# Kernel optimization log

Measured on AMD Instinct MI355X. Metric: run time of the kernel, lower is better.

The kernel has to match this reference:

```python
import jax, jax.numpy as jnp
import numpy as np

MAX_ONSET_DELAY_SAMPLES = 10


def apply_delays(templates, delays):
    # templates: (E, F, L), delays: (E, F) -> shifted templates with zero fill
    E, F, L = templates.shape
    d = jnp.round(jnp.clip(delays, -MAX_ONSET_DELAY_SAMPLES, MAX_ONSET_DELAY_SAMPLES)).astype(jnp.int32)
    idx = jnp.arange(L)                                   # (L,)
    src = idx[None, None, :] - d[:, :, None]              # (E, F, L) source index for torch.roll(shift=d)
    valid = (src >= 0) & (src < L)                        # zero out wrapped-around region
    src_c = jnp.clip(src, 0, L - 1)
    shifted = jnp.take_along_axis(templates, src_c, axis=2)
    return jnp.where(valid, shifted, jnp.zeros((), templates.dtype))


def setup_inputs() -> dict:
    key = jax.random.key(0)
    k1, k2, k3 = jax.random.split(key, 3)
    B, S, F = 64, 32768, 6
    E, L = 16, 80
    x = jax.random.normal(k1, (B, S, F), dtype=jnp.float32)
    templates = jax.random.normal(k2, (E, F, L), dtype=jnp.float32) * 0.1
    onset_delays = jax.random.normal(k3, (E, F), dtype=jnp.float32)
    return {"x": x, "templates": templates, "onset_delays": onset_delays}


def reference(x, templates, onset_delays):
    # x: (B, S, F); templates: (E, F, L); onset_delays: (E, F) -> scores (B, S, E)
    B, S, F = x.shape
    E, _, L = templates.shape
    delayed = apply_delays(templates, onset_delays)       # (E, F, L)
    kern = jnp.flip(delayed, axis=2)                      # torch flips template before conv1d
    pad = (L - 1) // 2
    # Fuse the 96 per-(event,feature) conv1d calls into one conv: sum over features
    # is exactly the input-channel contraction of a dense conv1d (in=F, out=E).
    score = jax.lax.conv_general_dilated(
        jnp.transpose(x, (0, 2, 1)),                      # (B, F, S)
        kern,                                             # (E, F, L) as OIH
        window_strides=(1,),
        padding=[(pad, pad)],
        dimension_numbers=("NCH", "OIH", "NCH"),
    )                                                     # (B, E, S_out)
    S_out = score.shape[2]
    if S_out > S:
        score = score[:, :, :S]
    elif S_out < S:
        score = jnp.pad(score, ((0, 0), (0, 0), (0, S - S_out)))
    return jnp.transpose(score, (0, 2, 1)) / (L * F)      # (B, S, E)
```

## Files before the change

### kernel.cpp

```cpp
#include <hip/hip_runtime.h>

#define BB 64
#define SS 32768
#define FF 6
#define EE 16
#define LL 80
#define KK 480
#define NSL 15
#define TBLK 256
#define NPHI 4
#define WROW 332
#define WUNITS 166

typedef _Float16 half8 __attribute__((ext_vector_type(8)));
typedef float f32x4 __attribute__((ext_vector_type(4)));

__global__ void prep_kernel(const float* __restrict__ tpl, const float* __restrict__ dly,
                            _Float16* __restrict__ wrev) {
    int n = blockIdx.x * 256 + threadIdx.x;
    if (n >= EE * KK) return;
    int e = n / KK, k = n - e * KK;
    int f = k / LL, r = k - f * LL;
    int m = LL - 1 - r;
    float dl = fminf(fmaxf(dly[e * FF + f], -10.f), 10.f);
    int d = (int)rintf(dl);
    int src = m - d;
    float v = (src >= 0 && src < LL) ? tpl[(e * FF + f) * LL + src] : 0.f;
    wrev[n] = (_Float16)v;
}

template <bool FROM_WS>
__global__ __launch_bounds__(256, 4) void corr_kernel(
    const float* __restrict__ x, const float* __restrict__ tpl,
    const float* __restrict__ dly, const _Float16* __restrict__ wrev,
    float* __restrict__ out) {
    __shared__ alignas(16) _Float16 xs[NPHI][FF][WROW];

    int tid = threadIdx.x;
    int b = blockIdx.x >> 7;
    int t0 = (blockIdx.x & 127) << 8;

    int lane = tid & 63;
    int wid = tid >> 6;
    int e = lane & 15;
    int g = lane >> 4;

    const float* xb = x + (size_t)b * (SS * FF);
    for (int it = tid; it < NPHI * WUNITS; it += 256) {
        int phi = it / WUNITS;
        int i = (it - phi * WUNITS) * 2;
        int pos = t0 + phi - 39 + i;
        float va[12];
        if (pos >= 0 && pos <= SS - 2) {
            const float* xp = xb + (size_t)pos * FF;
            #pragma unroll
            for (int q = 0; q < 6; q++)
                *(float2*)&va[2 * q] = *(const float2*)&xp[2 * q];
        } else {
            #pragma unroll
            for (int q = 0; q < 2; q++) {
                int p = pos + q;
                bool ok = (p >= 0) && (p < SS);
                #pragma unroll
                for (int f = 0; f < FF; f++)
                    va[q * 6 + f] = ok ? xb[(size_t)p * FF + f] : 0.f;
            }
        }
        #pragma unroll
        for (int f = 0; f < FF; f++) {
#if __has_builtin(__builtin_amdgcn_cvt_pkrtz)
            __fp16 __attribute__((ext_vector_type(2))) hp =
                __builtin_amdgcn_cvt_pkrtz(va[f], va[6 + f]);
            *(decltype(hp)*)&xs[phi][f][i] = hp;
#else
            xs[phi][f][i] = (_Float16)va[f];
            xs[phi][f][i + 1] = (_Float16)va[6 + f];
#endif
        }
    }

    f32x4 bqv[NSL];
    if constexpr (FROM_WS) {
        #pragma unroll
        for (int s = 0; s < NSL; s++)
            bqv[s] = *(const f32x4*)&wrev[e * KK + 32 * s + 8 * g];
    } else {
        __shared__ _Float16 Wlds[EE * KK];
        for (int n = tid; n < EE * KK; n += 256) {
            int ee = n / KK, k = n - ee * KK;
            int f = k / LL, r = k - f * LL;
            int m = LL - 1 - r;
            float dl = fminf(fmaxf(dly[ee * FF + f], -10.f), 10.f);
            int d = (int)rintf(dl);
            int src = m - d;
            float v = (src >= 0 && src < LL) ? tpl[(ee * FF + f) * LL + src] : 0.f;
            Wlds[n] = (_Float16)v;
        }
        __syncthreads();
        #pragma unroll
        for (int s = 0; s < NSL; s++)
            bqv[s] = *(const f32x4*)&Wlds[e * KK + 32 * s + 8 * g];
    }
    #pragma unroll
    for (int s = 0; s < NSL; s++)
        asm volatile("" : "+v"(bqv[s]));

    __syncthreads();

    int phi = wid;
    const char* xph = (const char*)&xs[phi][0][0];
    f32x4 acc[4];
    #pragma unroll
    for (int tt = 0; tt < 4; tt++) acc[tt] = (f32x4){0.f, 0.f, 0.f, 0.f};

    #pragma unroll
    for (int tt = 0; tt < 4; tt++) {
        int R = tt * 16 + (lane & 15);
        #pragma unroll
        for (int s = 0; s < NSL; s++) {
            int k0 = 32 * s + 8 * g;
            int f = (k0 * 205) >> 14;
            int r0 = k0 - 80 * f;
            const char* p = xph + 2 * (f * WROW + 4 * R + r0);
            uint2 lo = *(const uint2*)p;
            uint2 hi = *(const uint2*)(p + 8);
            union { unsigned u[4]; half8 h; } av;
            av.u[0] = lo.x; av.u[1] = lo.y; av.u[2] = hi.x; av.u[3] = hi.y;
            union { f32x4 f4; half8 h; } bv;
            bv.f4 = bqv[s];
            acc[tt] = __builtin_amdgcn_mfma_f32_16x16x32_f16(av.h, bv.h, acc[tt], 0, 0, 0);
        }
    }

    #pragma unroll
    for (int tt = 0; tt < 4; tt++) {
        #pragma unroll
        for (int j = 0; j < 4; j++) {
            int row = tt * 16 + g * 4 + j;
            int t = t0 + phi + 4 * row;
            float v = acc[tt][j] * (1.0f / 480.0f);
            if (t == SS - 1) v = 0.f;
            out[((size_t)b * SS + t) * EE + e] = v;
        }
    }
}

extern "C" void kernel_launch(void* const* d_in, const int* in_sizes, int n_in,
                              void* d_out, int out_size, void* d_ws, size_t ws_size,
                              hipStream_t stream) {
    const float* x = (const float*)d_in[0];
    const float* tpl = (const float*)d_in[1];
    const float* dly = (const float*)d_in[2];
    float* out = (float*)d_out;

    int grid = BB * (SS / TBLK);
    if (ws_size >= (size_t)(EE * KK * sizeof(_Float16))) {
        _Float16* wrev = (_Float16*)d_ws;
        prep_kernel<<<(EE * KK + 255) / 256, 256, 0, stream>>>(tpl, dly, wrev);
        corr_kernel<true><<<grid, 256, 0, stream>>>(x, tpl, dly, wrev, out);
    } else {
        corr_kernel<false><<<grid, 256, 0, stream>>>(x, tpl, dly, nullptr, out);
    }
}
```

Before: 68.26 us.

## Process four time tiles per block with per-wave private staging, no block barriers

Each block now covers 1024 time steps by looping over four 256-step tiles, so the per-block weight load into registers is amortized over four times as much work, and the grid shrinks by the same factor. Each wave loads and converts only its own phase slice of x into shared memory, which removes both __syncthreads barriers. The fallback path builds the weight fragments directly in registers instead of through a shared-memory table. Risks are fewer blocks and less parallelism across the GPU, serialized load-then-compute inside each wave with no overlap, and some lanes loading clamped duplicate rows.

```diff
diff --git a/kernel.cpp b/kernel.cpp
--- a/kernel.cpp
+++ b/kernel.cpp
@@ -8,12 +8,13 @@
 #define KK 480
 #define NSL 15
 #define TBLK 256
+#define NT 4
 #define NPHI 4
 #define WROW 332
-#define WUNITS 166
 
 typedef _Float16 half8 __attribute__((ext_vector_type(8)));
 typedef float f32x4 __attribute__((ext_vector_type(4)));
+typedef __fp16 h2 __attribute__((ext_vector_type(2)));
 
 __global__ void prep_kernel(const float* __restrict__ tpl, const float* __restrict__ dly,
                             _Float16* __restrict__ wrev) {
@@ -37,47 +38,15 @@
     __shared__ alignas(16) _Float16 xs[NPHI][FF][WROW];
 
     int tid = threadIdx.x;
-    int b = blockIdx.x >> 7;
-    int t0 = (blockIdx.x & 127) << 8;
-
     int lane = tid & 63;
-    int wid = tid >> 6;
+    int w = tid >> 6;
     int e = lane & 15;
     int g = lane >> 4;
 
+    int b = blockIdx.x >> 5;
+    int T0 = (blockIdx.x & 31) << 10;
+
     const float* xb = x + (size_t)b * (SS * FF);
-    for (int it = tid; it < NPHI * WUNITS; it += 256) {
-        int phi = it / WUNITS;
-        int i = (it - phi * WUNITS) * 2;
-        int pos = t0 + phi - 39 + i;
-        float va[12];
-        if (pos >= 0 && pos <= SS - 2) {
-            const float* xp = xb + (size_t)pos * FF;
-            #pragma unroll
-            for (int q = 0; q < 6; q++)
-                *(float2*)&va[2 * q] = *(const float2*)&xp[2 * q];
-        } else {
-            #pragma unroll
-            for (int q = 0; q < 2; q++) {
-                int p = pos + q;
-                bool ok = (p >= 0) && (p < SS);
-                #pragma unroll
-                for (int f = 0; f < FF; f++)
-                    va[q * 6 + f] = ok ? xb[(size_t)p * FF + f] : 0.f;
-            }
-        }
-        #pragma unroll
-        for (int f = 0; f < FF; f++) {
-#if __has_builtin(__builtin_amdgcn_cvt_pkrtz)
-            __fp16 __attribute__((ext_vector_type(2))) hp =
-                __builtin_amdgcn_cvt_pkrtz(va[f], va[6 + f]);
-            *(decltype(hp)*)&xs[phi][f][i] = hp;
-#else
-            xs[phi][f][i] = (_Float16)va[f];
-            xs[phi][f][i + 1] = (_Float16)va[6 + f];
-#endif
-        }
-    }
 
     f32x4 bqv[NSL];
     if constexpr (FROM_WS) {
@@ -85,62 +54,103 @@
         for (int s = 0; s < NSL; s++)
             bqv[s] = *(const f32x4*)&wrev[e * KK + 32 * s + 8 * g];
     } else {
-        __shared__ _Float16 Wlds[EE * KK];
-        for (int n = tid; n < EE * KK; n += 256) {
-            int ee = n / KK, k = n - ee * KK;
-            int f = k / LL, r = k - f * LL;
-            int m = LL - 1 - r;
-            float dl = fminf(fmaxf(dly[ee * FF + f], -10.f), 10.f);
-            int d = (int)rintf(dl);
-            int src = m - d;
-            float v = (src >= 0 && src < LL) ? tpl[(ee * FF + f) * LL + src] : 0.f;
-            Wlds[n] = (_Float16)v;
+        #pragma unroll
+        for (int s = 0; s < NSL; s++) {
+            union { f32x4 f4; _Float16 h[8]; } u;
+            #pragma unroll
+            for (int j = 0; j < 8; j++) {
+                int k = 32 * s + 8 * g + j;
+                int f = k / LL, r = k - f * LL;
+                int m = LL - 1 - r;
+                float dl = fminf(fmaxf(dly[e * FF + f], -10.f), 10.f);
+                int d = (int)rintf(dl);
+                int src = m - d;
+                u.h[j] = (_Float16)((src >= 0 && src < LL) ? tpl[(e * FF + f) * LL + src] : 0.f);
+            }
+            bqv[s] = u.f4;
         }
-        __syncthreads();
-        #pragma unroll
-        for (int s = 0; s < NSL; s++)
-            bqv[s] = *(const f32x4*)&Wlds[e * KK + 32 * s + 8 * g];
     }
     #pragma unroll
     for (int s = 0; s < NSL; s++)
         asm volatile("" : "+v"(bqv[s]));
 
-    __syncthreads();
+    _Float16* xsw = &xs[w][0][0];
 
-    int phi = wid;
-    const char* xph = (const char*)&xs[phi][0][0];
-    f32x4 acc[4];
-    #pragma unroll
-    for (int tt = 0; tt < 4; tt++) acc[tt] = (f32x4){0.f, 0.f, 0.f, 0.f};
+    for (int i = 0; i < NT; i++) {
+        int t0 = T0 + (i << 8);
+        int pbase = t0 + w - 39;
 
-    #pragma unroll
-    for (int tt = 0; tt < 4; tt++) {
-        int R = tt * 16 + (lane & 15);
+        float va[3][12];
+        bool edge = (pbase < 0) | (pbase + 331 >= SS);
+        if (!edge) {
+            #pragma unroll
+            for (int c = 0; c < 3; c++) {
+                int pi = lane + 64 * c; if (pi > 165) pi = 165;
+                const float* xp = xb + (size_t)(pbase + 2 * pi) * FF;
+                #pragma unroll
+                for (int q = 0; q < 6; q++)
+                    *(float2*)&va[c][2 * q] = *(const float2*)&xp[2 * q];
+            }
+        } else {
+            #pragma unroll
+            for (int c = 0; c < 3; c++) {
+                int pi = lane + 64 * c; if (pi > 165) pi = 165;
+                int pos = pbase + 2 * pi;
+                #pragma unroll
+                for (int q = 0; q < 2; q++) {
+                    int p = pos + q;
+                    bool ok = (p >= 0) && (p < SS);
+                    #pragma unroll
+                    for (int f = 0; f < FF; f++)
+                        va[c][q * 6 + f] = ok ? xb[(size_t)p * FF + f] : 0.f;
+                }
+            }
+        }
         #pragma unroll
-        for (int s = 0; s < NSL; s++) {
-            int k0 = 32 * s + 8 * g;
-            int f = (k0 * 205) >> 14;
-            int r0 = k0 - 80 * f;
-            const char* p = xph + 2 * (f * WROW + 4 * R + r0);
-            uint2 lo = *(const uint2*)p;
-            uint2 hi = *(const uint2*)(p + 8);
-            union { unsigned u[4]; half8 h; } av;
-            av.u[0] = lo.x; av.u[1] = lo.y; av.u[2] = hi.x; av.u[3] = hi.y;
-            union { f32x4 f4; half8 h; } bv;
-            bv.f4 = bqv[s];
-            acc[tt] = __builtin_amdgcn_mfma_f32_16x16x32_f16(av.h, bv.h, acc[tt], 0, 0, 0);
+        for (int c = 0; c < 3; c++) {
+            int pi = lane + 64 * c;
+            if (pi < 166) {
+                #pragma unroll
+                for (int f = 0; f < FF; f++) {
+                    h2 hp = __builtin_amdgcn_cvt_pkrtz(va[c][f], va[c][6 + f]);
+                    *(h2*)&xsw[f * WROW + 2 * pi] = hp;
+                }
+            }
         }
-    }
 
-    #pragma unroll
-    for (int tt = 0; tt < 4; tt++) {
+        f32x4 acc[4];
         #pragma unroll
-        for (int j = 0; j < 4; j++) {
-            int row = tt * 16 + g * 4 + j;
-            int t = t0 + phi + 4 * row;
-            float v = acc[tt][j] * (1.0f / 480.0f);
-            if (t == SS - 1) v = 0.f;
-            out[((size_t)b * SS + t) * EE + e] = v;
+        for (int tt = 0; tt < 4; tt++) acc[tt] = (f32x4){0.f, 0.f, 0.f, 0.f};
+        const char* xph = (const char*)xsw;
+        #pragma unroll
+        for (int tt = 0; tt < 4; tt++) {
+            int R = tt * 16 + e;
+            #pragma unroll
+            for (int s = 0; s < NSL; s++) {
+                int k0 = 32 * s + 8 * g;
+                int f = (k0 * 205) >> 14;
+                int r0 = k0 - 80 * f;
+                const char* p = xph + 2 * (f * WROW + 4 * R + r0);
+                uint2 lo = *(const uint2*)p;
+                uint2 hi = *(const uint2*)(p + 8);
+                union { unsigned u[4]; half8 h; } av;
+                av.u[0] = lo.x; av.u[1] = lo.y; av.u[2] = hi.x; av.u[3] = hi.y;
+                union { f32x4 f4; half8 h; } bv;
+                bv.f4 = bqv[s];
+                acc[tt] = __builtin_amdgcn_mfma_f32_16x16x32_f16(av.h, bv.h, acc[tt], 0, 0, 0);
+            }
+        }
+
+        #pragma unroll
+        for (int tt = 0; tt < 4; tt++) {
+            #pragma unroll
+            for (int j = 0; j < 4; j++) {
+                int row = tt * 16 + g * 4 + j;
+                int t = t0 + w + 4 * row;
+                float v = acc[tt][j] * (1.0f / 480.0f);
+                if (t == SS - 1) v = 0.f;
+                out[((size_t)b * SS + t) * EE + e] = v;
+            }
         }
     }
 }
@@ -153,7 +163,7 @@
     const float* dly = (const float*)d_in[2];
     float* out = (float*)d_out;
 
-    int grid = BB * (SS / TBLK);
+    int grid = BB * (SS / (TBLK * NT));
     if (ws_size >= (size_t)(EE * KK * sizeof(_Float16))) {
         _Float16* wrev = (_Float16*)d_ws;
         prep_kernel<<<(EE * KK + 255) / 256, 256, 0, stream>>>(tpl, dly, wrev);
```

Result: slower. 148.9 us (+118.2%).

## Halve block to two waves, each covering all four phases over half the rows

Applied to the files above, without the earlier changes.

Blocks go from four waves to two. Each wave now loops over all four phase slices and handles 32 of the 64 rows, instead of one wave per phase. The weight-fragment load is moved ahead of the x staging so it overlaps the staging work, and the per-unit bounds test is replaced by a block-level edge flag. The LDS row stride is padded from 332 to 336. The fallback path now builds weights straight into registers instead of going through LDS. Each thread now does twice the staging work and the MFMA work runs serially across phases, which trades parallelism per block for lower per-block overhead.

```diff
diff --git a/kernel.cpp b/kernel.cpp
--- a/kernel.cpp
+++ b/kernel.cpp
@@ -9,11 +9,13 @@
 #define NSL 15
 #define TBLK 256
 #define NPHI 4
-#define WROW 332
-#define WUNITS 166
+#define WROW 336
+#define UPP 166
+#define NUNITS 664
 
 typedef _Float16 half8 __attribute__((ext_vector_type(8)));
 typedef float f32x4 __attribute__((ext_vector_type(4)));
+typedef __fp16 h2 __attribute__((ext_vector_type(2)));
 
 __global__ void prep_kernel(const float* __restrict__ tpl, const float* __restrict__ dly,
                             _Float16* __restrict__ wrev) {
@@ -30,28 +32,56 @@
 }
 
 template <bool FROM_WS>
-__global__ __launch_bounds__(256, 4) void corr_kernel(
+__global__ __launch_bounds__(128, 4) void corr_kernel(
     const float* __restrict__ x, const float* __restrict__ tpl,
     const float* __restrict__ dly, const _Float16* __restrict__ wrev,
     float* __restrict__ out) {
     __shared__ alignas(16) _Float16 xs[NPHI][FF][WROW];
 
     int tid = threadIdx.x;
+    int lane = tid & 63;
+    int w = tid >> 6;
+    int e = lane & 15;
+    int g = lane >> 4;
+
     int b = blockIdx.x >> 7;
     int t0 = (blockIdx.x & 127) << 8;
 
-    int lane = tid & 63;
-    int wid = tid >> 6;
-    int e = lane & 15;
-    int g = lane >> 4;
+    const float* xb = x + (size_t)b * (SS * FF);
 
-    const float* xb = x + (size_t)b * (SS * FF);
-    for (int it = tid; it < NPHI * WUNITS; it += 256) {
-        int phi = it / WUNITS;
-        int i = (it - phi * WUNITS) * 2;
-        int pos = t0 + phi - 39 + i;
+    f32x4 bqv[NSL];
+    if constexpr (FROM_WS) {
+        #pragma unroll
+        for (int s = 0; s < NSL; s++)
+            bqv[s] = *(const f32x4*)&wrev[e * KK + 32 * s + 8 * g];
+    } else {
+        #pragma unroll
+        for (int s = 0; s < NSL; s++) {
+            union { f32x4 f4; _Float16 h[8]; } u;
+            #pragma unroll
+            for (int j = 0; j < 8; j++) {
+                int k = 32 * s + 8 * g + j;
+                int f = k / LL, r = k - f * LL;
+                int m = LL - 1 - r;
+                float dl = fminf(fmaxf(dly[e * FF + f], -10.f), 10.f);
+                int d = (int)rintf(dl);
+                int src = m - d;
+                u.h[j] = (_Float16)((src >= 0 && src < LL) ? tpl[(e * FF + f) * LL + src] : 0.f);
+            }
+            bqv[s] = u.f4;
+        }
+    }
+    #pragma unroll
+    for (int s = 0; s < NSL; s++)
+        asm volatile("" : "+v"(bqv[s]));
+
+    bool edge = (t0 - 39 < 0) | (t0 + 296 > SS);
+    for (int u = tid; u < NUNITS; u += 128) {
+        int phi = u / UPP;
+        int i2 = (u - phi * UPP) * 2;
+        int pos = t0 + phi - 39 + i2;
         float va[12];
-        if (pos >= 0 && pos <= SS - 2) {
+        if (!edge) {
             const float* xp = xb + (size_t)pos * FF;
             #pragma unroll
             for (int q = 0; q < 6; q++)
@@ -68,79 +98,41 @@
         }
         #pragma unroll
         for (int f = 0; f < FF; f++) {
-#if __has_builtin(__builtin_amdgcn_cvt_pkrtz)
-            __fp16 __attribute__((ext_vector_type(2))) hp =
-                __builtin_amdgcn_cvt_pkrtz(va[f], va[6 + f]);
-            *(decltype(hp)*)&xs[phi][f][i] = hp;
-#else
-            xs[phi][f][i] = (_Float16)va[f];
-            xs[phi][f][i + 1] = (_Float16)va[6 + f];
-#endif
+            h2 hp = __builtin_amdgcn_cvt_pkrtz(va[f], va[6 + f]);
+            *(h2*)&xs[phi][f][i2] = hp;
         }
     }
-
-    f32x4 bqv[NSL];
-    if constexpr (FROM_WS) {
-        #pragma unroll
-        for (int s = 0; s < NSL; s++)
-            bqv[s] = *(const f32x4*)&wrev[e * KK + 32 * s + 8 * g];
-    } else {
-        __shared__ _Float16 Wlds[EE * KK];
-        for (int n = tid; n < EE * KK; n += 256) {
-            int ee = n / KK, k = n - ee * KK;
-            int f = k / LL, r = k - f * LL;
-            int m = LL - 1 - r;
-            float dl = fminf(fmaxf(dly[ee * FF + f], -10.f), 10.f);
-            int d = (int)rintf(dl);
-            int src = m - d;
-            float v = (src >= 0 && src < LL) ? tpl[(ee * FF + f) * LL + src] : 0.f;
-            Wlds[n] = (_Float16)v;
-        }
-        __syncthreads();
-        #pragma unroll
-        for (int s = 0; s < NSL; s++)
-            bqv[s] = *(const f32x4*)&Wlds[e * KK + 32 * s + 8 * g];
-    }
-    #pragma unroll
-    for (int s = 0; s < NSL; s++)
-        asm volatile("" : "+v"(bqv[s]));
-
     __syncthreads();
 
-    int phi = wid;
-    const char* xph = (const char*)&xs[phi][0][0];
-    f32x4 acc[4];
     #pragma unroll
-    for (int tt = 0; tt < 4; tt++) acc[tt] = (f32x4){0.f, 0.f, 0.f, 0.f};
-
-    #pragma unroll
-    for (int tt = 0; tt < 4; tt++) {
-        int R = tt * 16 + (lane & 15);
+    for (int phi = 0; phi < NPHI; phi++) {
+        const char* xph = (const char*)&xs[phi][0][0];
         #pragma unroll
-        for (int s = 0; s < NSL; s++) {
-            int k0 = 32 * s + 8 * g;
-            int f = (k0 * 205) >> 14;
-            int r0 = k0 - 80 * f;
-            const char* p = xph + 2 * (f * WROW + 4 * R + r0);
-            uint2 lo = *(const uint2*)p;
-            uint2 hi = *(const uint2*)(p + 8);
-            union { unsigned u[4]; half8 h; } av;
-            av.u[0] = lo.x; av.u[1] = lo.y; av.u[2] = hi.x; av.u[3] = hi.y;
-            union { f32x4 f4; half8 h; } bv;
-            bv.f4 = bqv[s];
-            acc[tt] = __builtin_amdgcn_mfma_f32_16x16x32_f16(av.h, bv.h, acc[tt], 0, 0, 0);
-        }
-    }
-
-    #pragma unroll
-    for (int tt = 0; tt < 4; tt++) {
-        #pragma unroll
-        for (int j = 0; j < 4; j++) {
-            int row = tt * 16 + g * 4 + j;
-            int t = t0 + phi + 4 * row;
-            float v = acc[tt][j] * (1.0f / 480.0f);
-            if (t == SS - 1) v = 0.f;
-            out[((size_t)b * SS + t) * EE + e] = v;
+        for (int tt = 0; tt < 2; tt++) {
+            int R = 32 * w + 16 * tt + e;
+            f32x4 acc = {0.f, 0.f, 0.f, 0.f};
+            #pragma unroll
+            for (int s = 0; s < NSL; s++) {
+                int k0 = 32 * s + 8 * g;
+                int f = (k0 * 205) >> 14;
+                int r0 = k0 - 80 * f;
+                const char* p = xph + 2 * (f * WROW + 4 * R + r0);
+                uint2 lo = *(const uint2*)p;
+                uint2 hi = *(const uint2*)(p + 8);
+                union { unsigned u[4]; half8 h; } av;
+                av.u[0] = lo.x; av.u[1] = lo.y; av.u[2] = hi.x; av.u[3] = hi.y;
+                union { f32x4 f4; half8 h; } bv;
+                bv.f4 = bqv[s];
+                acc = __builtin_amdgcn_mfma_f32_16x16x32_f16(av.h, bv.h, acc, 0, 0, 0);
+            }
+            #pragma unroll
+            for (int j = 0; j < 4; j++) {
+                int row = 32 * w + 16 * tt + g * 4 + j;
+                int t = t0 + phi + 4 * row;
+                float v = acc[j] * (1.0f / 480.0f);
+                if (t == SS - 1) v = 0.f;
+                out[((size_t)b * SS + t) * EE + e] = v;
+            }
         }
     }
 }
@@ -157,8 +149,8 @@
     if (ws_size >= (size_t)(EE * KK * sizeof(_Float16))) {
         _Float16* wrev = (_Float16*)d_ws;
         prep_kernel<<<(EE * KK + 255) / 256, 256, 0, stream>>>(tpl, dly, wrev);
-        corr_kernel<true><<<grid, 256, 0, stream>>>(x, tpl, dly, wrev, out);
+        corr_kernel<true><<<grid, 128, 0, stream>>>(x, tpl, dly, wrev, out);
     } else {
-        corr_kernel<false><<<grid, 256, 0, stream>>>(x, tpl, dly, nullptr, out);
+        corr_kernel<false><<<grid, 128, 0, stream>>>(x, tpl, dly, nullptr, out);
     }
 }
```

Result: slower. 73.97 us (+8.4%).
